# Kernel optimization log

Measured on AMD Instinct MI355X. Metric: run time of the kernel, lower is better.

Reference implementation:

```python
import jax, jax.numpy as jnp
import numpy as np
from jax.scipy.special import logsumexp

B, T, LD, HD, K = 64, 2048, 16, 64, 8
TEMP = 1.0  # annealing=False
LOG2PI = float(np.log(2.0 * np.pi))


def setup_inputs() -> dict:
    key = jax.random.key(0)
    ks = jax.random.split(key, 10)
    return {
        "z": jax.random.normal(ks[0], (B, T, LD), jnp.float32),
        "pi": jax.random.normal(ks[1], (K,), jnp.float32) * 0.5,
        "Q": jax.random.normal(ks[2], (K, K), jnp.float32) * 0.5,
        "init_mean": jax.random.normal(ks[3], (K, LD), jnp.float32),
        # torch init: rand(K,1,1) * eye(LD) * 5  (a scale factor per state)
        "init_cov": jax.random.uniform(ks[4], (K, 1, 1), jnp.float32) * 5.0 * jnp.eye(LD, dtype=jnp.float32)[None],
        "covs": jnp.tile(jnp.eye(LD, dtype=jnp.float32)[None], (K, 1, 1)) + 0.05 * jax.random.normal(ks[5], (K, LD, LD), jnp.float32),
        "W1": jax.random.normal(ks[6], (K, HD, LD), jnp.float32) / np.sqrt(LD),
        "b1": jnp.zeros((K, HD), jnp.float32),
        "W2": jax.random.normal(ks[7], (K, LD, HD), jnp.float32) / np.sqrt(HD),
        "b2": jnp.zeros((K, LD), jnp.float32),
    }


def _chol_terms(C):
    """Sigma = C C^T + 1e-6 I ; return (L^{-1}, 0.5*logdet) per state."""
    dim = C.shape[-1]
    Sigma = C @ jnp.swapaxes(C, -1, -2) + 1e-6 * jnp.eye(dim, dtype=C.dtype)
    L = jnp.linalg.cholesky(Sigma)  # [K,D,D]
    Linv = jax.vmap(lambda l: jax.scipy.linalg.solve_triangular(l, jnp.eye(dim, dtype=C.dtype), lower=True))(L)
    logdet_half = jnp.sum(jnp.log(jnp.diagonal(L, axis1=-2, axis2=-1)), -1)  # [K]
    return Linv, logdet_half


def _mvn_logp(diff, Linv, logdet_half):
    # diff [B,t,K,D], Linv [K,D,D] -> [B,t,K]
    y = jnp.einsum('kde,btke->btkd', Linv, diff)
    maha = jnp.sum(y * y, -1)
    d = diff.shape[-1]
    return -0.5 * maha - logdet_half - 0.5 * d * LOG2PI


def reference(z, pi, Q, init_mean, init_cov, covs, W1, b1, W2, b2):
    # ---- local evidence: log p(z_1|s_1), log p(z_t | z_{t-1}, s_t)  [B,T,K]
    Linv0, ld0 = _chol_terms(init_cov)
    le1 = _mvn_logp(z[:, :1, None, :] - init_mean, Linv0, ld0)  # [B,1,K]
    zp = z[:, :-1]  # [B,T-1,D]
    h = jax.nn.softplus(jnp.einsum('btd,khd->btkh', zp, W1) + b1)  # per-state MLP hidden
    mu = jnp.einsum('btkh,kdh->btkd', h, W2) + b2  # [B,T-1,K,D]
    LinvT, ldT = _chol_terms(covs)
    leT = _mvn_logp(z[:, 1:, None, :] - mu, LinvT, ldT)  # [B,T-1,K]
    le = jnp.concatenate([le1, leT], axis=1)  # [B,T,K]

    # ---- alpha recursion (filtering)
    logpi = jax.nn.log_softmax(pi / TEMP)
    Qlog = jax.nn.log_softmax(Q / TEMP, axis=-1)  # log p(s_t=j | s_{t-1}=i)
    QT = Qlog.T  # [to, from]
    lp0 = le[:, 0] + logpi
    lz0 = logsumexp(lp0, -1)
    la0 = lp0 - lz0[:, None]
    le_rest = jnp.swapaxes(le[:, 1:], 0, 1)  # [T-1,B,K]

    def astep(la_prev, le_t):
        lp = logsumexp(le_t[:, :, None] + QT[None] + la_prev[:, None, :], axis=-1)
        lz = logsumexp(lp, -1)
        la = lp - lz[:, None]
        return la, (la, lz)

    _, (las, lzs) = jax.lax.scan(astep, la0, le_rest)
    log_alpha = jnp.concatenate([la0[:, None], jnp.swapaxes(las, 0, 1)], axis=1)  # [B,T,K]
    log_Z = jnp.concatenate([lz0[:, None], lzs.T], axis=1)  # [B,T]

    # ---- beta recursion (smoothing), reverse scan
    def bstep(lb_next, inp):
        le_t, lz_t = inp
        lb = logsumexp(Qlog[None] + le_t[:, None, :] + lb_next[:, None, :], axis=-1) - lz_t[:, None]
        return lb, lb

    _, lbs = jax.lax.scan(bstep, jnp.zeros((B, K), le.dtype), (le_rest, log_Z[:, 1:].T), reverse=True)
    log_beta = jnp.concatenate([jnp.swapaxes(lbs, 0, 1), jnp.zeros((B, 1, K), le.dtype)], axis=1)

    # ---- posteriors
    gamma = jnp.exp(log_alpha + log_beta)  # [B,T,K]
    paired = jnp.exp(Qlog[None, None] + log_alpha[:, :-1, :, None] + log_beta[:, 1:, None, :] + le[:, 1:, None, :] - log_Z[:, 1:, None, None])  # [B,T-1,K,K]
    return gamma, paired, log_Z
```

## Files before the change

### kernel.cpp

```cpp
#include <hip/hip_runtime.h>

#define B_ 64
#define T_ 2048
#define LD_ 16
#define HD_ 64
#define K_ 8
#define L_ 16
#define C_ 128
#define S_ 16

constexpr int OFF_LE    = 0;
constexpr int OFF_ALPHA = 1048576;
constexpr int OFF_EBAR  = 2097152;
constexpr int OFF_ZT    = OFF_ALPHA;
constexpr int OFF_PBUF  = 3145728;
constexpr int OFF_RLOG  = 3670016;
constexpr int OFF_SBUF  = 3809280;
constexpr int OFF_UBUF  = 3874816;
constexpr int OFF_ULOG  = 3940352;
constexpr int OFF_SAIN  = 3941376;
constexpr int OFF_BENT  = 3949568;
constexpr int OFF_PRM   = 3957760;

constexpr int P_LINV0 = 0;
constexpr int P_LINVT = 2048;
constexpr int P_LD0   = 4096;
constexpr int P_LDT   = 4104;
constexpr int P_LOGPI = 4112;
constexpr int P_QEXP  = 4120;
constexpr int P_QTEXP = 4184;
constexpr int P_QTV   = 4256;
constexpr int P_QV    = 4768;

constexpr int FI_NC2 = 32768;
constexpr int FI_C0I = 32896;

constexpr int OUT_PAIRED = B_*T_*K_;
constexpr int OUT_LOGZ   = OUT_PAIRED + B_*(T_-1)*K_*K_;

template<int CTRL>
__device__ __forceinline__ float dppmov(float x) {
  int xi = __float_as_int(x);
  int r = __builtin_amdgcn_update_dpp(xi, xi, CTRL, 0xF, 0xF, true);
  return __int_as_float(r);
}
__device__ __forceinline__ void allg8(float v, float w[8]) {
  w[0] = v;
  w[1] = dppmov<0xB1>(v);
  w[2] = dppmov<0x4E>(v);
  w[3] = dppmov<0x4E>(w[1]);
  w[7] = dppmov<0x141>(v);
  w[6] = dppmov<0xB1>(w[7]);
  w[5] = dppmov<0x4E>(w[7]);
  w[4] = dppmov<0x4E>(w[6]);
}
template<int V> __device__ __forceinline__ float xorg8(float x);
template<> __device__ __forceinline__ float xorg8<0>(float x) { return x; }
template<> __device__ __forceinline__ float xorg8<1>(float x) { return dppmov<0xB1>(x); }
template<> __device__ __forceinline__ float xorg8<2>(float x) { return dppmov<0x4E>(x); }
template<> __device__ __forceinline__ float xorg8<3>(float x) { return dppmov<0x4E>(dppmov<0xB1>(x)); }
template<> __device__ __forceinline__ float xorg8<4>(float x) { return dppmov<0x4E>(dppmov<0xB1>(dppmov<0x141>(x))); }
template<> __device__ __forceinline__ float xorg8<5>(float x) { return dppmov<0x4E>(dppmov<0x141>(x)); }
template<> __device__ __forceinline__ float xorg8<6>(float x) { return dppmov<0xB1>(dppmov<0x141>(x)); }
template<> __device__ __forceinline__ float xorg8<7>(float x) { return dppmov<0x141>(x); }

__device__ __forceinline__ float bfly_sum8(float x) {
  x += dppmov<0xB1>(x); x += dppmov<0x4E>(x); x += dppmov<0x141>(x); return x;
}
__device__ __forceinline__ float bfly_max8(float x) {
  x = fmaxf(x, dppmov<0xB1>(x)); x = fmaxf(x, dppmov<0x4E>(x)); x = fmaxf(x, dppmov<0x141>(x)); return x;
}
__device__ __forceinline__ float rcpnr(float x) {
  float r0 = __builtin_amdgcn_rcpf(x);
  return r0 * __builtin_fmaf(-x, r0, 2.0f);
}
__device__ __forceinline__ void absg8(float v, float w[8]) {
  int x = __float_as_int(v);
  w[0] = __int_as_float(__builtin_amdgcn_ds_swizzle(x, 0x18));
  w[1] = __int_as_float(__builtin_amdgcn_ds_swizzle(x, 0x38));
  w[2] = __int_as_float(__builtin_amdgcn_ds_swizzle(x, 0x58));
  w[3] = __int_as_float(__builtin_amdgcn_ds_swizzle(x, 0x78));
  w[4] = __int_as_float(__builtin_amdgcn_ds_swizzle(x, 0x98));
  w[5] = __int_as_float(__builtin_amdgcn_ds_swizzle(x, 0xB8));
  w[6] = __int_as_float(__builtin_amdgcn_ds_swizzle(x, 0xD8));
  w[7] = __int_as_float(__builtin_amdgcn_ds_swizzle(x, 0xF8));
}
__device__ __forceinline__ void col2row(const float cl[8], float rv[8]) {
  rv[0] = cl[0];
  rv[1] = xorg8<1>(cl[1]);
  rv[2] = xorg8<2>(cl[2]);
  rv[3] = xorg8<3>(cl[3]);
  rv[4] = xorg8<4>(cl[4]);
  rv[5] = xorg8<5>(cl[5]);
  rv[6] = xorg8<6>(cl[6]);
  rv[7] = xorg8<7>(cl[7]);
}
__device__ __forceinline__ void mmul8(const float a[8], const float m[8], float o[8]) {
  float m8[8][8];
  #pragma unroll
  for (int w = 0; w < 8; w++) allg8(m[w], m8[w]);
  #pragma unroll
  for (int v = 0; v < 8; v++) {
    float acc = 0.f;
    #pragma unroll
    for (int u = 0; u < 8; u++) acc = __builtin_fmaf(a[u], m8[u^v][u], acc);
    o[v] = acc;
  }
}
__device__ __forceinline__ float maxnorm8(float m[8]) {
  float mx = m[0];
  #pragma unroll
  for (int u = 1; u < 8; u++) mx = fmaxf(mx, m[u]);
  mx = bfly_max8(mx);
  float r = rcpnr(mx);
  #pragma unroll
  for (int u = 0; u < 8; u++) m[u] *= r;
  return mx;
}
__device__ __forceinline__ void load_rows(const float* p, float r[8]) {
  const float4* q = (const float4*)p;
  float4 x0 = q[0], x1 = q[1];
  r[0]=x0.x; r[1]=x0.y; r[2]=x0.z; r[3]=x0.w;
  r[4]=x1.x; r[5]=x1.y; r[6]=x1.z; r[7]=x1.w;
}
__device__ __forceinline__ void load16(const float* p, float r[16]) {
  const float4* q = (const float4*)p;
  float4 a0=q[0], a1=q[1], a2=q[2], a3=q[3];
  r[0]=a0.x; r[1]=a0.y; r[2]=a0.z; r[3]=a0.w;
  r[4]=a1.x; r[5]=a1.y; r[6]=a1.z; r[7]=a1.w;
  r[8]=a2.x; r[9]=a2.y; r[10]=a2.z; r[11]=a2.w;
  r[12]=a3.x; r[13]=a3.y; r[14]=a3.z; r[15]=a3.w;
}
__device__ __forceinline__ void store16(float* p, const float r[16]) {
  float4* q = (float4*)p;
  q[0] = make_float4(r[0],r[1],r[2],r[3]);
  q[1] = make_float4(r[4],r[5],r[6],r[7]);
  q[2] = make_float4(r[8],r[9],r[10],r[11]);
  q[3] = make_float4(r[12],r[13],r[14],r[15]);
}
__device__ __forceinline__ float dotw8(const float r[8], const float w[8]) {
  return ((r[0]*w[0]+r[1]*w[1]) + (r[2]*w[2]+r[3]*w[3]))
       + ((r[4]*w[4]+r[5]*w[5]) + (r[6]*w[6]+r[7]*w[7]));
}

typedef __attribute__((ext_vector_type(4))) float f32x4;
typedef __attribute__((ext_vector_type(8))) short bf16x8;

__device__ __forceinline__ unsigned ph(float a, float b) {
  return (__float_as_uint(a) >> 16) | (__float_as_uint(b) & 0xFFFF0000u);
}
__device__ __forceinline__ float hif(float a) {
  return __uint_as_float(__float_as_uint(a) & 0xFFFF0000u);
}
__device__ __forceinline__ bf16x8 u2f(uint4 u) {
  return __builtin_bit_cast(bf16x8, u);
}
__device__ __forceinline__ uint4 mkfrag_u4(float4 v) {
  unsigned ux = __float_as_uint(v.x), uy = __float_as_uint(v.y);
  unsigned uz = __float_as_uint(v.z), uw = __float_as_uint(v.w);
  unsigned h01 = (ux >> 16) | (uy & 0xFFFF0000u);
  unsigned h23 = (uz >> 16) | (uw & 0xFFFF0000u);
  float lx = v.x - __uint_as_float(ux & 0xFFFF0000u);
  float ly = v.y - __uint_as_float(uy & 0xFFFF0000u);
  float lz = v.z - __uint_as_float(uz & 0xFFFF0000u);
  float lw = v.w - __uint_as_float(uw & 0xFFFF0000u);
  unsigned l01 = ph(lx, ly);
  unsigned l23 = ph(lz, lw);
  return make_uint4(h01, h23, l01, l23);
}
__device__ __forceinline__ f32x4 MF(bf16x8 a, bf16x8 b, f32x4 c) {
  return __builtin_amdgcn_mfma_f32_16x16x32_bf16(a, b, c, 0, 0, 0);
}

__global__ __launch_bounds__(64) void prep_kernel(
    const float* __restrict__ pi, const float* __restrict__ Q,
    const float* __restrict__ init_cov, const float* __restrict__ covs,
    float* __restrict__ prm)
{
  int tid = threadIdx.x;
  int blk = blockIdx.x;
  if (blk < 16) {
    int k = blk & 7;
    const float* C = (blk < 8 ? init_cov : covs) + k*256;
    float* outL  = prm + (blk < 8 ? P_LINV0 : P_LINVT) + k*256;
    float* outld = prm + (blk < 8 ? P_LD0   : P_LDT)   + k;
    __shared__ float S[16][17], L[16][17], X[16][17];
    for (int e = tid; e < 256; e += 64) {
      int r = e >> 4, c = e & 15;
      float s = (r == c) ? 1e-6f : 0.f;
      for (int l = 0; l < 16; l++) s += C[r*16+l] * C[c*16+l];
      S[r][c] = s;
    }
    __syncthreads();
    for (int j = 0; j < 16; j++) {
      if (tid == 0) L[j][j] = sqrtf(S[j][j]);
      __syncthreads();
      if (tid > j && tid < 16) L[tid][j] = S[tid][j] / L[j][j];
      __syncthreads();
      if (tid > j && tid < 16) {
        float ltj = L[tid][j];
        for (int c = j+1; c <= tid; c++) S[tid][c] -= ltj * L[c][j];
      }
      __syncthreads();
    }
    if (tid < 16) {
      int c = tid;
      for (int r = 0; r < 16; r++) {
        float v;
        if (r < c) v = 0.f;
        else {
          v = (r == c) ? 1.f : 0.f;
          for (int s2 = c; s2 < r; s2++) v -= L[r][s2] * X[s2][c];
          v /= L[r][r];
        }
        X[r][c] = v;
      }
    }
    __syncthreads();
    for (int e = tid; e < 256; e += 64) outL[e] = X[e>>4][e&15];
    if (tid == 0) {
      float ld = 0.f;
      for (int j = 0; j < 16; j++) ld += logf(L[j][j]);
      *outld = ld;
    }
  } else {
    if (tid < 8) {
      int row = tid;
      float q[8], mx = -1e30f;
      for (int j = 0; j < 8; j++) { q[j] = Q[row*8+j]; mx = fmaxf(mx, q[j]); }
      float s = 0.f;
      for (int j = 0; j < 8; j++) s += __expf(q[j]-mx);
      float ls = logf(s);
      for (int j = 0; j < 8; j++) {
        float e = __expf(q[j]-mx-ls);
        prm[P_QEXP  + row*8 + j] = e;
        prm[P_QTEXP + j*8 + row] = e;
      }
    } else if (tid == 8) {
      float p[8], mx = -1e30f;
      for (int j = 0; j < 8; j++) { p[j] = pi[j]; mx = fmaxf(mx, p[j]); }
      float s = 0.f;
      for (int j = 0; j < 8; j++) s += __expf(p[j]-mx);
      float ls = logf(s);
      for (int j = 0; j < 8; j++) prm[P_LOGPI+j] = p[j]-mx-ls;
    }
  }
}

__global__ __launch_bounds__(64) void prep2_kernel(
    const float* __restrict__ W1, const float* __restrict__ W2,
    const float* __restrict__ b2, const float* __restrict__ init_mean,
    float* __restrict__ prm, float* __restrict__ frag)
{
  int k = blockIdx.x, tid = threadIdx.x;
  if (k == 0) {
    int j = tid >> 3, x = tid & 7;
    for (int v = 0; v < 8; v++) {
      prm[P_QTV + j*64 + x*8 + v] = prm[P_QTEXP + (j^x)*8 + (j^v)];
      prm[P_QV  + j*64 + x*8 + v] = prm[P_QEXP  + (j^x)*8 + (j^v)];
    }
  }
  __shared__ float Ls[16][16], L0s[16][16], G[16][64];
  for (int e = tid; e < 256; e += 64) {
    Ls[e>>4][e&15]  = prm[P_LINVT + k*256 + e];
    L0s[e>>4][e&15] = prm[P_LINV0 + k*256 + e];
  }
  __syncthreads();
  for (int idx = tid; idx < 1024; idx += 64) {
    int d = idx >> 6, hh = idx & 63;
    float s = 0.f;
    for (int e = 0; e < 16; e++) s += Ls[d][e] * W2[k*1024 + e*64 + hh];
    G[d][hh] = -s;
  }
  __syncthreads();
  int d = tid & 15, q = tid >> 4;
  uint4* F4 = (uint4*)frag;
  for (int kc = 0; kc < 2; kc++) {
    float v[8], lo[8];
    for (int j = 0; j < 8; j++) {
      int hh = 32*kc + 16*(j>>2) + 4*q + (j&3);
      v[j] = G[d][hh];
      lo[j] = v[j] - hif(v[j]);
    }
    F4[6144 + ((k*2+kc)*4+q)*16 + d] =
        make_uint4(ph(v[0],v[1]), ph(v[2],v[3]), ph(v[4],v[5]), ph(v[6],v[7]));
    F4[7168 + ((k*2+kc)*4+q)*16 + d] =
        make_uint4(ph(lo[0],lo[1]), ph(lo[2],lo[3]), ph(lo[4],lo[5]), ph(lo[6],lo[7]));
  }
  for (int mt = 0; mt < 4; mt++) {
    int hh = 16*mt + d;
    float v[4], lo[4];
    for (int j = 0; j < 4; j++) { v[j] = W1[k*1024 + hh*16 + 4*q + j]; lo[j] = v[j] - hif(v[j]); }
    unsigned x = ph(v[0],v[1]), y = ph(v[2],v[3]);
    F4[((k*4+mt)*4+q)*16 + d]        = make_uint4(x, y, x, y);
    F4[2048 + ((k*4+mt)*4+q)*16 + d] = make_uint4(ph(lo[0],lo[1]), ph(lo[2],lo[3]), 0u, 0u);
  }
  {
    float v[4], lo[4];
    for (int j = 0; j < 4; j++) { v[j] = Ls[d][4*q+j]; lo[j] = v[j] - hif(v[j]); }
    unsigned x = ph(v[0],v[1]), y = ph(v[2],v[3]);
    F4[4096 + (k*4+q)*16 + d] = make_uint4(x, y, x, y);
    F4[4608 + (k*4+q)*16 + d] = make_uint4(ph(lo[0],lo[1]), ph(lo[2],lo[3]), 0u, 0u);
    for (int j = 0; j < 4; j++) { v[j] = L0s[d][4*q+j]; lo[j] = v[j] - hif(v[j]); }
    x = ph(v[0],v[1]); y = ph(v[2],v[3]);
    F4[5120 + (k*4+q)*16 + d] = make_uint4(x, y, x, y);
    F4[5632 + (k*4+q)*16 + d] = make_uint4(ph(lo[0],lo[1]), ph(lo[2],lo[3]), 0u, 0u);
  }
  if (q == 0) {
    float s2 = 0.f, s0 = 0.f;
    for (int e = 0; e < 16; e++) {
      s2 += Ls[d][e]  * b2[k*16+e];
      s0 += L0s[d][e] * init_mean[k*16+e];
    }
    frag[FI_NC2 + k*16 + d] = -s2;
    frag[FI_C0I + k*16 + d] = -s0;
  }
}

__global__ __launch_bounds__(256) void ztr_kernel(
    const float* __restrict__ z, uint4* __restrict__ zf)
{
  int tid = blockIdx.x*256 + threadIdx.x;
  int t = tid >> 6, b = tid & 63;
  const float4* src = (const float4*)(z + (b*T_ + t)*LD_);
  #pragma unroll
  for (int q = 0; q < 4; q++)
    zf[(t*4 + q)*64 + b] = mkfrag_u4(src[q]);
}

__global__ __launch_bounds__(256) void emisB_kernel(
    const uint4* __restrict__ zf, const float* __restrict__ b1,
    const float* __restrict__ frag, const float* __restrict__ prm,
    float* __restrict__ lebuf)
{
  int lane = threadIdx.x & 63;
  int wid = __builtin_amdgcn_readfirstlane(blockIdx.x*4 + (threadIdx.x >> 6));
  int bblk = wid & 3;
  int tch  = (wid >> 2) & 255;
  int k    = wid >> 10;
  int c = lane & 15, q = lane >> 4;
  int b = bblk*16 + c;
  const uint4* F4 = (const uint4*)frag;

  bf16x8 w1a1[4], w1a2[4];
  #pragma unroll
  for (int mt = 0; mt < 4; mt++) {
    w1a1[mt] = u2f(F4[((k*4+mt)*4+q)*16 + c]);
    w1a2[mt] = u2f(F4[2048 + ((k*4+mt)*4+q)*16 + c]);
  }
  bf16x8 lva1 = u2f(F4[4096 + (k*4+q)*16 + c]);
  bf16x8 lva2 = u2f(F4[4608 + (k*4+q)*16 + c]);
  bf16x8 gahi[2], galo[2];
  #pragma unroll
  for (int kc = 0; kc < 2; kc++) {
    gahi[kc] = u2f(F4[6144 + ((k*2+kc)*4+q)*16 + c]);
    galo[kc] = u2f(F4[7168 + ((k*2+kc)*4+q)*16 + c]);
  }
  float b1iv[16];
  #pragma unroll
  for (int i = 0; i < 16; i++)
    b1iv[i] = b1[k*64 + (i>>2)*16 + 4*q + (i&3)];
  float nc2[4];
  #pragma unroll
  for (int r = 0; r < 4; r++) nc2[r] = frag[FI_NC2 + k*16 + 4*q + r];
  float lconst = -prm[P_LDT + k] - 14.70301653f;

  int t0 = tch*8;
  bf16x8 zp;
  int ttstart;
  if (tch == 0) {
    bf16x8 zc0 = u2f(zf[q*64 + b]);
    bf16x8 l0a1 = u2f(F4[5120 + (k*4+q)*16 + c]);
    bf16x8 l0a2 = u2f(F4[5632 + (k*4+q)*16 + c]);
    f32x4 acc;
    acc[0] = frag[FI_C0I + k*16 + 4*q + 0];
    acc[1] = frag[FI_C0I + k*16 + 4*q + 1];
    acc[2] = frag[FI_C0I + k*16 + 4*q + 2];
    acc[3] = frag[FI_C0I + k*16 + 4*q + 3];
    acc = MF(l0a1, zc0, acc);
    acc = MF(l0a2, zc0, acc);
    float m2 = (acc[0]*acc[0] + acc[1]*acc[1]) + (acc[2]*acc[2] + acc[3]*acc[3]);
    m2 += __shfl_xor(m2, 16);
    m2 += __shfl_xor(m2, 32);
    float le = -0.5f*m2 - prm[P_LD0+k] - 14.70301653f + prm[P_LOGPI+k];
    if (q == 0) lebuf[(b*8 + k)*16] = le;
    zp = zc0;
    ttstart = 1;
  } else {
    zp = u2f(zf[((t0-1)*4 + q)*64 + b]);
    ttstart = 0;
  }

  uint4 zvu = zf[((t0+ttstart)*4 + q)*64 + b];
  #pragma unroll 1
  for (int tt = ttstart; tt < 8; tt++) {
    int t = t0 + tt;
    uint4 zvn = zvu;
    if (tt < 7) zvn = zf[((t+1)*4 + q)*64 + b];
    bf16x8 zc = u2f(zvu);
    f32x4 a1[4];
    #pragma unroll
    for (int mt = 0; mt < 4; mt++) {
      f32x4 ai;
      ai[0] = b1iv[mt*4+0]; ai[1] = b1iv[mt*4+1];
      ai[2] = b1iv[mt*4+2]; ai[3] = b1iv[mt*4+3];
      ai = MF(w1a1[mt], zp, ai);
      a1[mt] = MF(w1a2[mt], zp, ai);
    }
    float hv[16];
    #pragma unroll
    for (int i = 0; i < 16; i++) {
      float a = a1[i>>2][i&3];
      hv[i] = __logf(1.f + __expf(a));
    }
    bf16x8 hhi[2], hlo[2];
    #pragma unroll
    for (int kc = 0; kc < 2; kc++) {
      const float* hp = hv + 8*kc;
      hhi[kc] = u2f(make_uint4(ph(hp[0],hp[1]), ph(hp[2],hp[3]),
                               ph(hp[4],hp[5]), ph(hp[6],hp[7])));
      float l0 = hp[0]-hif(hp[0]), l1 = hp[1]-hif(hp[1]);
      float l2 = hp[2]-hif(hp[2]), l3 = hp[3]-hif(hp[3]);
      float l4 = hp[4]-hif(hp[4]), l5 = hp[5]-hif(hp[5]);
      float l6 = hp[6]-hif(hp[6]), l7 = hp[7]-hif(hp[7]);
      hlo[kc] = u2f(make_uint4(ph(l0,l1), ph(l2,l3), ph(l4,l5), ph(l6,l7)));
    }
    f32x4 acc;
    acc[0] = nc2[0]; acc[1] = nc2[1]; acc[2] = nc2[2]; acc[3] = nc2[3];
    acc = MF(lva1, zc, acc);
    acc = MF(lva2, zc, acc);
    #pragma unroll
    for (int kc = 0; kc < 2; kc++) {
      acc = MF(gahi[kc], hhi[kc], acc);
      acc = MF(galo[kc], hhi[kc], acc);
      acc = MF(gahi[kc], hlo[kc], acc);
    }
    float m2 = (acc[0]*acc[0] + acc[1]*acc[1]) + (acc[2]*acc[2] + acc[3]*acc[3]);
    m2 += __shfl_xor(m2, 16);
    m2 += __shfl_xor(m2, 32);
    float le = -0.5f*m2 + lconst;
    if (q == 0) lebuf[(((t>>4)*64 + b)*8 + k)*16 + (t&15)] = le;
    zp = zc;
    zvu = zvn;
  }
}

__global__ __launch_bounds__(256) void fwdA_kernel(
    const float* __restrict__ lebuf, const float* __restrict__ prm,
    float* __restrict__ pbuf, float* __restrict__ sbuf)
{
  int lane64 = threadIdx.x & 63;
  int iu = threadIdx.x >> 6;
  int unit = blockIdx.x*4 + iu;
  int b = unit & 63, s = unit >> 6;
  int u = lane64 >> 3, j = lane64 & 7;
  int c = 8*s + u;
  float qtv[64];
  load16(prm + P_QTV + j*64,      qtv);
  load16(prm + P_QTV + j*64 + 16, qtv+16);
  load16(prm + P_QTV + j*64 + 32, qtv+32);
  load16(prm + P_QTV + j*64 + 48, qtv+48);
  float lev[16];
  load16(lebuf + ((c*64 + b)*8 + j)*16, lev);
  float pl[8];
  if (c == 0) {
    float m = bfly_max8(lev[0]);
    float e = __expf(lev[0]-m);
    allg8(e, pl);
  } else {
    float m = bfly_max8(lev[0]);
    float e = __expf(lev[0]-m);
    float e8[8]; allg8(e, e8);
    float np[8];
    #pragma unroll
    for (int x = 0; x < 8; x++) np[x] = e8[x] * qtv[x*8];
    float mx = np[0];
    #pragma unroll
    for (int x = 1; x < 8; x++) mx = fmaxf(mx, np[x]);
    mx = bfly_max8(mx);
    float r = rcpnr(mx);
    #pragma unroll
    for (int x = 0; x < 8; x++) pl[x] = np[x] * r;
  }
  #pragma unroll
  for (int sx = 1; sx < 16; sx++) {
    float m = bfly_max8(lev[sx]);
    float e = __expf(lev[sx]-m);
    float e8[8]; allg8(e, e8);
    float np[8];
    #pragma unroll
    for (int x = 0; x < 8; x++) {
      float acc = 0.f;
      #pragma unroll
      for (int v = 0; v < 8; v++) acc = __builtin_fmaf(qtv[x*8+v], pl[v], acc);
      np[x] = e8[x] * acc;
    }
    float mx = np[0];
    #pragma unroll
    for (int x = 1; x < 8; x++) mx = fmaxf(mx, np[x]);
    mx = bfly_max8(mx);
    float r = rcpnr(mx);
    #pragma unroll
    for (int x = 0; x < 8; x++) pl[x] = np[x] * r;
  }
  float rv[8]; col2row(pl, rv);
  float4* dst = (float4*)(pbuf + (c*64 + b)*64 + j*8);
  dst[0] = make_float4(rv[0], rv[1], rv[2], rv[3]);
  dst[1] = make_float4(rv[4], rv[5], rv[6], rv[7]);
  __shared__ float M[4][8][64];
  #pragma unroll
  for (int v = 0; v < 8; v++) M[iu][u][j*8+v] = rv[v];
  __syncthreads();
  if (u == 0) {
    float m[8];
    #pragma unroll
    for (int v = 0; v < 8; v++) m[v] = M[iu][0][j*8+v];
    for (int cc = 1; cc < 8; cc++) {
      float a[8];
      #pragma unroll
      for (int v = 0; v < 8; v++) a[v] = M[iu][cc][j*8+v];
      float nm[8];
      mmul8(a, m, nm);
      maxnorm8(nm);
      #pragma unroll
      for (int v = 0; v < 8; v++) m[v] = nm[v];
    }
    float4* d2 = (float4*)(sbuf + (s*64 + b)*64 + j*8);
    d2[0] = make_float4(m[0], m[1], m[2], m[3]);
    d2[1] = make_float4(m[4], m[5], m[6], m[7]);
  }
}

__global__ __launch_bounds__(512) void fwdP2b_kernel(
    const float* __restrict__ sbuf, float* __restrict__ sain)
{
  int lane = threadIdx.x;
  int b = lane >> 3, i = lane & 7;
  const float4* base = (const float4*)sbuf;
  float4 c0 = base[(0*64+b)*16 + i*2], c1 = base[(0*64+b)*16 + i*2 + 1];
  float a = 0.125f;
  for (int s = 0; s < 16; s++) {
    int s2 = (s < 15) ? s+1 : 15;
    float4 n0 = base[(s2*64+b)*16 + i*2], n1 = base[(s2*64+b)*16 + i*2 + 1];
    float aw[8]; allg8(a, aw);
    float sm = ((c0.x*aw[0] + c0.y*aw[1]) + (c0.z*aw[2] + c0.w*aw[3]))
             + ((c1.x*aw[4] + c1.y*aw[5]) + (c1.z*aw[6] + c1.w*aw[7]));
    float tot = bfly_sum8(sm);
    float an = sm * rcpnr(tot);
    if (s < 15) { a = an; sain[(s+1)*512 + b*8 + i] = a; }
    c0 = n0; c1 = n1;
  }
}

__global__ __launch_bounds__(256) void fwdB_kernel(
    const float* __restrict__ lebuf, const float* __restrict__ prm,
    const float* __restrict__ sain, float* pbuf,
    float* __restrict__ alpha, float* __restrict__ ebar,
    float* __restrict__ rlog, float* __restrict__ ubuf,
    float* __restrict__ ulog, float* __restrict__ out)
{
  int lane64 = threadIdx.x & 63;
  int iu = threadIdx.x >> 6;
  int unit = blockIdx.x*4 + iu;
  int b = unit & 63, s = unit >> 6;
  int u = lane64 >> 3, i = lane64 & 7;
  int c = 8*s + u;
  int off = b*8 + i;
  __shared__ float Als[4][8];
  __shared__ float Mh[4][8][64];
  __shared__ float Lh[4][8];
  float pr[8];
  load_rows(pbuf + (c*64 + b)*64 + i*8, pr);
  float lev[16];
  load16(lebuf + ((c*64 + b)*8 + i)*16, lev);
  float av_in = 0.f;
  if (u == 0) av_in = (s == 0) ? 0.125f : sain[s*512 + off];
  for (int r = 0; r < 7; r++) {
    if (u == r) {
      if (r > 0) av_in = Als[iu][i];
      float aw[8]; allg8(av_in, aw);
      float sm = dotw8(pr, aw);
      float tot = bfly_sum8(sm);
      Als[iu][i] = sm * rcpnr(tot);
    }
    __syncthreads();
  }
  if (u == 7) av_in = Als[iu][i];
  float q[8];
  #pragma unroll
  for (int x = 0; x < 8; x++) q[x] = prm[P_QTEXP + i*8 + (i^x)];
  float* logZ = out + OUT_LOGZ + b*T_;
  float av_arr[16], eb_loc[16];
  float a;
  if (c == 0) {
    float m0 = bfly_max8(lev[0]);
    float e0x = __expf(lev[0]-m0);
    float ct = bfly_sum8(e0x);
    float rr = rcpnr(ct);
    a = e0x * rr;
    av_arr[0] = a;
    eb_loc[0] = a;
    if (i == 0) logZ[0] = m0 + __logf(ct);
  } else {
    a = av_in;
    float m = bfly_max8(lev[0]);
    float e = __expf(lev[0]-m);
    float w[8]; allg8(a, w);
    float dot = dotw8(q, w);
    float p = e * dot;
    float ct = bfly_sum8(p);
    float rr = rcpnr(ct);
    a = p * rr;
    av_arr[0] = a;
    eb_loc[0] = e * rr;
    if (i == 0) logZ[c*L_] = m + __logf(ct);
  }
  #pragma unroll
  for (int x = 1; x < 16; x++) {
    float m = bfly_max8(lev[x]);
    float e = __expf(lev[x]-m);
    float w[8]; allg8(a, w);
    float dot = dotw8(q, w);
    float p = e * dot;
    float ct = bfly_sum8(p);
    float rr = rcpnr(ct);
    a = p * rr;
    av_arr[x] = a;
    eb_loc[x] = e * rr;
    if (i == 0) logZ[c*L_ + x] = m + __logf(ct);
  }
  store16(alpha + ((c*64 + b)*8 + i)*16, av_arr);
  store16(ebar  + ((c*64 + b)*8 + i)*16, eb_loc);
  float qv[64];
  load16(prm + P_QV + i*64,      qv);
  load16(prm + P_QV + i*64 + 16, qv+16);
  load16(prm + P_QV + i*64 + 32, qv+32);
  load16(prm + P_QV + i*64 + 48, qv+48);
  float rl8[8];
  #pragma unroll
  for (int x = 0; x < 8; x++) rl8[x] = (x == 0) ? 1.f : 0.f;
  float lsc = 0.f;
  #pragma unroll
  for (int sx = 15; sx >= 1; sx--) {
    float e8[8]; allg8(eb_loc[sx], e8);
    float nr[8];
    #pragma unroll
    for (int x = 0; x < 8; x++) {
      float acc = 0.f;
      #pragma unroll
      for (int v = 0; v < 8; v++) acc = __builtin_fmaf(qv[x*8+v], e8[v]*rl8[v], acc);
      nr[x] = acc;
    }
    float mx = nr[0];
    #pragma unroll
    for (int x = 1; x < 8; x++) mx = fmaxf(mx, nr[x]);
    mx = bfly_max8(mx);
    float r = rcpnr(mx);
    #pragma unroll
    for (int x = 0; x < 8; x++) rl8[x] = nr[x] * r;
    lsc += __logf(mx);
  }
  float rv[8]; col2row(rl8, rv);
  float4* dstR = (float4*)(pbuf + (c*64 + b)*64 + i*8);
  dstR[0] = make_float4(rv[0], rv[1], rv[2], rv[3]);
  dstR[1] = make_float4(rv[4], rv[5], rv[6], rv[7]);
  if (i == 0) rlog[c*64 + b] = lsc;
  float qr[8];
  #pragma unroll
  for (int x = 0; x < 8; x++) qr[x] = prm[P_QEXP + i*8 + (i^x)];
  float d8[8];
  #pragma unroll
  for (int v = 0; v < 8; v++) d8[v] = eb_loc[0] * rv[v];
  float h8[8];
  mmul8(qr, d8, h8);
  float ls = lsc + __logf(maxnorm8(h8));
  #pragma unroll
  for (int v = 0; v < 8; v++) Mh[iu][u][i*8+v] = h8[v];
  if (i == 0) Lh[iu][u] = ls;
  __syncthreads();
  if (u == 0) {
    float m[8];
    #pragma unroll
    for (int v = 0; v < 8; v++) m[v] = Mh[iu][7][i*8+v];
    float lsum = Lh[iu][7];
    for (int cc = 6; cc >= 0; cc--) {
      float aa[8];
      #pragma unroll
      for (int v = 0; v < 8; v++) aa[v] = Mh[iu][cc][i*8+v];
      float t8[8];
      mmul8(aa, m, t8);
      lsum += Lh[iu][cc] + __logf(maxnorm8(t8));
      #pragma unroll
      for (int v = 0; v < 8; v++) m[v] = t8[v];
    }
    float4* d2 = (float4*)(ubuf + (s*64 + b)*64 + i*8);
    d2[0] = make_float4(m[0], m[1], m[2], m[3]);
    d2[1] = make_float4(m[4], m[5], m[6], m[7]);
    if (i == 0) ulog[s*64 + b] = lsum;
  }
}

__global__ __launch_bounds__(512) void bwdP2b_kernel(
    const float* __restrict__ ubuf, const float* __restrict__ ulog,
    float* __restrict__ bent)
{
  int lane = threadIdx.x;
  int b = lane >> 3, i = lane & 7;
  bent[15*512 + b*8 + i] = 1.f;
  const float4* base = (const float4*)ubuf;
  float sh = 1.f, sig = 0.f;
  float4 c0 = base[(15*64+b)*16 + i*2], c1 = base[(15*64+b)*16 + i*2 + 1];
  float cu = ulog[15*64 + b];
  for (int s = 15; s >= 1; s--) {
    int s2 = (s > 1) ? s-1 : 1;
    float4 n0 = base[(s2*64+b)*16 + i*2], n1 = base[(s2*64+b)*16 + i*2 + 1];
    float nu = ulog[s2*64 + b];
    float sw[8]; allg8(sh, sw);
    float y = ((c0.x*sw[0] + c0.y*sw[1]) + (c0.z*sw[2] + c0.w*sw[3]))
            + ((c1.x*sw[4] + c1.y*sw[5]) + (c1.z*sw[6] + c1.w*sw[7]));
    float mx = bfly_max8(y);
    sh = y * rcpnr(mx);
    sig += cu + __logf(mx);
    bent[(s-1)*512 + b*8 + i] = sh * __expf(sig);
    c0 = n0; c1 = n1; cu = nu;
  }
}

__global__ __launch_bounds__(256) void bwdC_kernel(
    const float* __restrict__ alpha, const float* __restrict__ ebar,
    const float* __restrict__ rbuf, const float* __restrict__ rlog,
    const float* __restrict__ prm, const float* __restrict__ bent,
    float* __restrict__ out)
{
  int lane64 = threadIdx.x & 63;
  int iu = threadIdx.x >> 6;
  int unit = blockIdx.x*4 + iu;
  int b = unit & 63, s = unit >> 6;
  int u = lane64 >> 3, i = lane64 & 7;
  int c = 8*s + u;
  int off = b*8 + i;
  float qr[8], qa[8];
  #pragma unroll
  for (int x = 0; x < 8; x++) qr[x] = prm[P_QEXP + i*8 + (i^x)];
  #pragma unroll
  for (int v = 0; v < 8; v++) qa[v] = prm[P_QEXP + i*8 + v];
  float r8[8];
  load_rows(rbuf + (c*64 + b)*64 + i*8, r8);
  float erl = __expf(rlog[c*64 + b]);
  int base = ((c*64 + b)*8 + i)*16;
  float av[16], ev[16];
  load16(alpha + base, av);
  load16(ebar  + base, ev);
  float e0 = ev[0];
  float avm1 = (c > 0) ? alpha[base - 8192 + 15] : 0.f;
  __shared__ float Bls[4][8];
  float bt = 0.f, y = 0.f, nbv = 0.f;
  for (int r = 7; r >= 0; r--) {
    if (u == r) {
      bt = (r == 7) ? bent[s*512 + off] : Bls[iu][i];
      float bw[8]; allg8(bt, bw);
      y = dotw8(r8, bw) * erl;
      float ey = e0 * y;
      float w[8]; allg8(ey, w);
      nbv = 0.f;
      #pragma unroll
      for (int v = 0; v < 8; v++) nbv = __builtin_fmaf(qr[v], w[v], nbv);
      if (r > 0) Bls[iu][i] = nbv;
    }
    __syncthreads();
  }
  float* po = out + OUT_PAIRED + b*((T_-1)*64);
  float* go = out + b*(T_*K_);
  float bb = bt;
  if (c == 127) go[2047*8 + i] = av[15];
  #pragma unroll
  for (int x = 15; x >= 1; x--) {
    float eya[8]; absg8(ev[x]*bb, eya);
    float term[8];
    #pragma unroll
    for (int v = 0; v < 8; v++) term[v] = qa[v]*eya[v];
    float nb = ((term[0]+term[1]) + (term[2]+term[3]))
             + ((term[4]+term[5]) + (term[6]+term[7]));
    int t = c*L_ + x - 1;
    float am = av[x-1];
    float4* pd = (float4*)(po + t*64 + i*8);
    pd[0] = make_float4(am*term[0], am*term[1], am*term[2], am*term[3]);
    pd[1] = make_float4(am*term[4], am*term[5], am*term[6], am*term[7]);
    go[t*8 + i] = am*nb;
    bb = nb;
  }
  if (c > 0) {
    float eya[8]; absg8(e0*y, eya);
    int t = c*L_ - 1;
    float4* pd = (float4*)(po + t*64 + i*8);
    pd[0] = make_float4(avm1*qa[0]*eya[0], avm1*qa[1]*eya[1],
                        avm1*qa[2]*eya[2], avm1*qa[3]*eya[3]);
    pd[1] = make_float4(avm1*qa[4]*eya[4], avm1*qa[5]*eya[5],
                        avm1*qa[6]*eya[6], avm1*qa[7]*eya[7]);
    go[t*8 + i] = avm1 * nbv;
  }
}

extern "C" void kernel_launch(void* const* d_in, const int* in_sizes, int n_in,
                              void* d_out, int out_size, void* d_ws, size_t ws_size,
                              hipStream_t stream) {
  const float* z         = (const float*)d_in[0];
  const float* pi        = (const float*)d_in[1];
  const float* Q         = (const float*)d_in[2];
  const float* init_mean = (const float*)d_in[3];
  const float* init_cov  = (const float*)d_in[4];
  const float* covs      = (const float*)d_in[5];
  const float* W1        = (const float*)d_in[6];
  const float* b1        = (const float*)d_in[7];
  const float* W2        = (const float*)d_in[8];
  const float* b2        = (const float*)d_in[9];
  float* out = (float*)d_out;
  float* ws  = (float*)d_ws;

  prep_kernel<<<17, 64, 0, stream>>>(pi, Q, init_cov, covs, ws + OFF_PRM);
  prep2_kernel<<<8, 64, 0, stream>>>(W1, W2, b2, init_mean, ws + OFF_PRM,
                                     ws + OFF_UBUF);
  ztr_kernel<<<512, 256, 0, stream>>>(z, (uint4*)(ws + OFF_ZT));
  emisB_kernel<<<2048, 256, 0, stream>>>((const uint4*)(ws + OFF_ZT), b1,
                                         ws + OFF_UBUF, ws + OFF_PRM,
                                         ws + OFF_LE);
  fwdA_kernel<<<256, 256, 0, stream>>>(ws + OFF_LE, ws + OFF_PRM,
                                       ws + OFF_PBUF, ws + OFF_SBUF);
  fwdP2b_kernel<<<1, 512, 0, stream>>>(ws + OFF_SBUF, ws + OFF_SAIN);
  fwdB_kernel<<<256, 256, 0, stream>>>(ws + OFF_LE, ws + OFF_PRM, ws + OFF_SAIN,
                                       ws + OFF_PBUF, ws + OFF_ALPHA,
                                       ws + OFF_EBAR, ws + OFF_RLOG,
                                       ws + OFF_UBUF, ws + OFF_ULOG, out);
  bwdP2b_kernel<<<1, 512, 0, stream>>>(ws + OFF_UBUF, ws + OFF_ULOG, ws + OFF_BENT);
  bwdC_kernel<<<256, 256, 0, stream>>>(ws + OFF_ALPHA, ws + OFF_EBAR,
                                       ws + OFF_PBUF, ws + OFF_RLOG,
                                       ws + OFF_PRM, ws + OFF_BENT, out);
}
```

Before: 264.4 us.

## Replace LDS-serialized chunk chains with wave shuffles and per-lane row matvecs

Rewrites the forward and backward 16-step chunk recursions to keep an 8-entry row of exp(Q) per lane and use mmul8 with DPP all-gathers, replacing the 64-float per-lane expanded transition tables. This drops the P_QTV/P_QV precompute in prep2 and the register pressure of those tables. The sequential 8-chunk combine loops in fwdB and bwdC now pass values between lane groups with __shfl instead of shared memory plus __syncthreads. Every lane group computes every step redundantly, which adds ALU work but removes barriers and idle lanes.

```diff
diff --git a/kernel.cpp b/kernel.cpp
--- a/kernel.cpp
+++ b/kernel.cpp
@@ -29,8 +29,6 @@
 constexpr int P_LOGPI = 4112;
 constexpr int P_QEXP  = 4120;
 constexpr int P_QTEXP = 4184;
-constexpr int P_QTV   = 4256;
-constexpr int P_QV    = 4768;
 
 constexpr int FI_NC2 = 32768;
 constexpr int FI_C0I = 32896;
@@ -96,15 +94,13 @@
   rv[7] = xorg8<7>(cl[7]);
 }
 __device__ __forceinline__ void mmul8(const float a[8], const float m[8], float o[8]) {
-  float m8[8][8];
-  #pragma unroll
-  for (int w = 0; w < 8; w++) allg8(m[w], m8[w]);
-  #pragma unroll
-  for (int v = 0; v < 8; v++) {
-    float acc = 0.f;
-    #pragma unroll
-    for (int u = 0; u < 8; u++) acc = __builtin_fmaf(a[u], m8[u^v][u], acc);
-    o[v] = acc;
+  #pragma unroll
+  for (int v = 0; v < 8; v++) o[v] = 0.f;
+  #pragma unroll
+  for (int w = 0; w < 8; w++) {
+    float w8[8]; allg8(m[w], w8);
+    #pragma unroll
+    for (int u = 0; u < 8; u++) o[u^w] = __builtin_fmaf(a[u], w8[u], o[u^w]);
   }
 }
 __device__ __forceinline__ float maxnorm8(float m[8]) {
@@ -250,16 +246,9 @@
 __global__ __launch_bounds__(64) void prep2_kernel(
     const float* __restrict__ W1, const float* __restrict__ W2,
     const float* __restrict__ b2, const float* __restrict__ init_mean,
-    float* __restrict__ prm, float* __restrict__ frag)
+    const float* __restrict__ prm, float* __restrict__ frag)
 {
   int k = blockIdx.x, tid = threadIdx.x;
-  if (k == 0) {
-    int j = tid >> 3, x = tid & 7;
-    for (int v = 0; v < 8; v++) {
-      prm[P_QTV + j*64 + x*8 + v] = prm[P_QTEXP + (j^x)*8 + (j^v)];
-      prm[P_QV  + j*64 + x*8 + v] = prm[P_QEXP  + (j^x)*8 + (j^v)];
-    }
-  }
   __shared__ float Ls[16][16], L0s[16][16], G[16][64];
   for (int e = tid; e < 256; e += 64) {
     Ls[e>>4][e&15]  = prm[P_LINVT + k*256 + e];
@@ -455,53 +444,37 @@
   int b = unit & 63, s = unit >> 6;
   int u = lane64 >> 3, j = lane64 & 7;
   int c = 8*s + u;
-  float qtv[64];
-  load16(prm + P_QTV + j*64,      qtv);
-  load16(prm + P_QTV + j*64 + 16, qtv+16);
-  load16(prm + P_QTV + j*64 + 32, qtv+32);
-  load16(prm + P_QTV + j*64 + 48, qtv+48);
+  float qrow[8];
+  #pragma unroll
+  for (int v = 0; v < 8; v++) qrow[v] = prm[P_QEXP + j*8 + (j^v)];
   float lev[16];
   load16(lebuf + ((c*64 + b)*8 + j)*16, lev);
   float pl[8];
-  if (c == 0) {
+  {
     float m = bfly_max8(lev[0]);
     float e = __expf(lev[0]-m);
-    allg8(e, pl);
-  } else {
-    float m = bfly_max8(lev[0]);
-    float e = __expf(lev[0]-m);
-    float e8[8]; allg8(e, e8);
-    float np[8];
-    #pragma unroll
-    for (int x = 0; x < 8; x++) np[x] = e8[x] * qtv[x*8];
-    float mx = np[0];
-    #pragma unroll
-    for (int x = 1; x < 8; x++) mx = fmaxf(mx, np[x]);
-    mx = bfly_max8(mx);
-    float r = rcpnr(mx);
-    #pragma unroll
-    for (int x = 0; x < 8; x++) pl[x] = np[x] * r;
+    if (c == 0) {
+      allg8(e, pl);
+    } else {
+      float e8[8]; allg8(e, e8);
+      #pragma unroll
+      for (int v = 0; v < 8; v++) pl[v] = qrow[v] * e8[v];
+      maxnorm8(pl);
+    }
   }
   #pragma unroll
   for (int sx = 1; sx < 16; sx++) {
     float m = bfly_max8(lev[sx]);
     float e = __expf(lev[sx]-m);
     float e8[8]; allg8(e, e8);
+    float mw[8];
+    #pragma unroll
+    for (int v = 0; v < 8; v++) mw[v] = qrow[v] * e8[v];
     float np[8];
-    #pragma unroll
-    for (int x = 0; x < 8; x++) {
-      float acc = 0.f;
-      #pragma unroll
-      for (int v = 0; v < 8; v++) acc = __builtin_fmaf(qtv[x*8+v], pl[v], acc);
-      np[x] = e8[x] * acc;
-    }
-    float mx = np[0];
-    #pragma unroll
-    for (int x = 1; x < 8; x++) mx = fmaxf(mx, np[x]);
-    mx = bfly_max8(mx);
-    float r = rcpnr(mx);
-    #pragma unroll
-    for (int x = 0; x < 8; x++) pl[x] = np[x] * r;
+    mmul8(pl, mw, np);
+    maxnorm8(np);
+    #pragma unroll
+    for (int v = 0; v < 8; v++) pl[v] = np[v];
   }
   float rv[8]; col2row(pl, rv);
   float4* dst = (float4*)(pbuf + (c*64 + b)*64 + j*8);
@@ -566,29 +539,26 @@
   int u = lane64 >> 3, i = lane64 & 7;
   int c = 8*s + u;
   int off = b*8 + i;
-  __shared__ float Als[4][8];
   __shared__ float Mh[4][8][64];
   __shared__ float Lh[4][8];
   float pr[8];
   load_rows(pbuf + (c*64 + b)*64 + i*8, pr);
   float lev[16];
   load16(lebuf + ((c*64 + b)*8 + i)*16, lev);
-  float av_in = 0.f;
-  if (u == 0) av_in = (s == 0) ? 0.125f : sain[s*512 + off];
+  float q[8];
+  #pragma unroll
+  for (int x = 0; x < 8; x++) q[x] = prm[P_QTEXP + i*8 + (i^x)];
+  float a_cur = (s == 0) ? 0.125f : sain[s*512 + off];
+  float av_in = a_cur;
+  #pragma unroll
   for (int r = 0; r < 7; r++) {
-    if (u == r) {
-      if (r > 0) av_in = Als[iu][i];
-      float aw[8]; allg8(av_in, aw);
-      float sm = dotw8(pr, aw);
-      float tot = bfly_sum8(sm);
-      Als[iu][i] = sm * rcpnr(tot);
-    }
-    __syncthreads();
-  }
-  if (u == 7) av_in = Als[iu][i];
-  float q[8];
-  #pragma unroll
-  for (int x = 0; x < 8; x++) q[x] = prm[P_QTEXP + i*8 + (i^x)];
+    float w[8]; allg8(a_cur, w);
+    float sm = dotw8(pr, w);
+    float tot = bfly_sum8(sm);
+    float an = sm * rcpnr(tot);
+    float as = __shfl(an, lane64 - 8);
+    if (u == r+1) { a_cur = as; av_in = as; }
+  }
   float* logZ = out + OUT_LOGZ + b*T_;
   float av_arr[16], eb_loc[16];
   float a;
@@ -631,34 +601,25 @@
   }
   store16(alpha + ((c*64 + b)*8 + i)*16, av_arr);
   store16(ebar  + ((c*64 + b)*8 + i)*16, eb_loc);
-  float qv[64];
-  load16(prm + P_QV + i*64,      qv);
-  load16(prm + P_QV + i*64 + 16, qv+16);
-  load16(prm + P_QV + i*64 + 32, qv+32);
-  load16(prm + P_QV + i*64 + 48, qv+48);
   float rl8[8];
-  #pragma unroll
-  for (int x = 0; x < 8; x++) rl8[x] = (x == 0) ? 1.f : 0.f;
-  float lsc = 0.f;
-  #pragma unroll
-  for (int sx = 15; sx >= 1; sx--) {
-    float e8[8]; allg8(eb_loc[sx], e8);
+  float lsc;
+  {
+    float e = eb_loc[15];
+    #pragma unroll
+    for (int v = 0; v < 8; v++) rl8[v] = e * q[v];
+    lsc = __logf(maxnorm8(rl8));
+  }
+  #pragma unroll
+  for (int sx = 14; sx >= 1; sx--) {
+    float e = eb_loc[sx];
+    float mw[8];
+    #pragma unroll
+    for (int v = 0; v < 8; v++) mw[v] = e * q[v];
     float nr[8];
-    #pragma unroll
-    for (int x = 0; x < 8; x++) {
-      float acc = 0.f;
-      #pragma unroll
-      for (int v = 0; v < 8; v++) acc = __builtin_fmaf(qv[x*8+v], e8[v]*rl8[v], acc);
-      nr[x] = acc;
-    }
-    float mx = nr[0];
-    #pragma unroll
-    for (int x = 1; x < 8; x++) mx = fmaxf(mx, nr[x]);
-    mx = bfly_max8(mx);
-    float r = rcpnr(mx);
-    #pragma unroll
-    for (int x = 0; x < 8; x++) rl8[x] = nr[x] * r;
-    lsc += __logf(mx);
+    mmul8(rl8, mw, nr);
+    lsc += __logf(maxnorm8(nr));
+    #pragma unroll
+    for (int v = 0; v < 8; v++) rl8[v] = nr[v];
   }
   float rv[8]; col2row(rl8, rv);
   float4* dstR = (float4*)(pbuf + (c*64 + b)*64 + i*8);
@@ -737,8 +698,8 @@
   int unit = blockIdx.x*4 + iu;
   int b = unit & 63, s = unit >> 6;
   int u = lane64 >> 3, i = lane64 & 7;
+  int off = b*8 + i;
   int c = 8*s + u;
-  int off = b*8 + i;
   float qr[8], qa[8];
   #pragma unroll
   for (int x = 0; x < 8; x++) qr[x] = prm[P_QEXP + i*8 + (i^x)];
@@ -753,25 +714,26 @@
   load16(ebar  + base, ev);
   float e0 = ev[0];
   float avm1 = (c > 0) ? alpha[base - 8192 + 15] : 0.f;
-  __shared__ float Bls[4][8];
-  float bt = 0.f, y = 0.f, nbv = 0.f;
+  float bt = bent[s*512 + off];
+  float bt_k = 0.f, y_k = 0.f, nbv_k = 0.f;
+  #pragma unroll
   for (int r = 7; r >= 0; r--) {
-    if (u == r) {
-      bt = (r == 7) ? bent[s*512 + off] : Bls[iu][i];
-      float bw[8]; allg8(bt, bw);
-      y = dotw8(r8, bw) * erl;
-      float ey = e0 * y;
-      float w[8]; allg8(ey, w);
-      nbv = 0.f;
-      #pragma unroll
-      for (int v = 0; v < 8; v++) nbv = __builtin_fmaf(qr[v], w[v], nbv);
-      if (r > 0) Bls[iu][i] = nbv;
-    }
-    __syncthreads();
+    float bw[8]; allg8(bt, bw);
+    float y = dotw8(r8, bw) * erl;
+    float ey = e0 * y;
+    float w[8]; allg8(ey, w);
+    float nbv = 0.f;
+    #pragma unroll
+    for (int v = 0; v < 8; v++) nbv = __builtin_fmaf(qr[v], w[v], nbv);
+    if (u == r) { bt_k = bt; y_k = y; nbv_k = nbv; }
+    if (r > 0) {
+      float bs = __shfl(nbv, lane64 + 8);
+      if (u == r-1) bt = bs;
+    }
   }
   float* po = out + OUT_PAIRED + b*((T_-1)*64);
   float* go = out + b*(T_*K_);
-  float bb = bt;
+  float bb = bt_k;
   if (c == 127) go[2047*8 + i] = av[15];
   #pragma unroll
   for (int x = 15; x >= 1; x--) {
@@ -790,14 +752,14 @@
     bb = nb;
   }
   if (c > 0) {
-    float eya[8]; absg8(e0*y, eya);
+    float eya[8]; absg8(e0*y_k, eya);
     int t = c*L_ - 1;
     float4* pd = (float4*)(po + t*64 + i*8);
     pd[0] = make_float4(avm1*qa[0]*eya[0], avm1*qa[1]*eya[1],
                         avm1*qa[2]*eya[2], avm1*qa[3]*eya[3]);
     pd[1] = make_float4(avm1*qa[4]*eya[4], avm1*qa[5]*eya[5],
                         avm1*qa[6]*eya[6], avm1*qa[7]*eya[7]);
-    go[t*8 + i] = avm1 * nbv;
+    go[t*8 + i] = avm1 * nbv_k;
   }
 }
 
```

Measured after the change: 276.3 us. +4.5%, slower.
